# Performance work log

Hardware: AMD Instinct MI355X
Metric: run time of the kernel (lower is better)

## Reference

```python
import jax, jax.numpy as jnp
import numpy as np

NOISE_STD = 0.05
ALPHA = 0.2
B, T, I, H, O = 64, 1000, 16, 512, 8


def setup_inputs() -> dict:
    key = jax.random.key(0)
    ks = jax.random.split(key, 5)
    x = jax.random.normal(ks[0], (B, T, I), dtype=jnp.float32)
    noise = jax.random.normal(ks[1], (B, T, H), dtype=jnp.float32)
    # parameter init mirrors torch: wi ~ N(0,1), wrec ~ N(0, rho/sqrt(H)), wo ~ N(0, 1/H)
    wi = jax.random.normal(ks[2], (I, H), dtype=jnp.float32)
    si = jnp.ones((I,), dtype=jnp.float32)
    wrec = jax.random.normal(ks[3], (H, H), dtype=jnp.float32) * (1.0 / np.sqrt(H))
    wo = jax.random.normal(ks[4], (H, O), dtype=jnp.float32) * (1.0 / H)
    so = jnp.ones((O,), dtype=jnp.float32)
    h0 = jnp.zeros((H,), dtype=jnp.float32)
    return {"x": x, "noise": noise, "wi": wi, "si": si, "wrec": wrec,
            "wo": wo, "so": so, "h0": h0}


def reference(x, noise, wi, si, wrec, wo, so, h0):
    # proxy params: wi_full = (wi.T * si).T ; wo_full = wo * so
    wi_full = si[:, None] * wi            # (I, H)
    wo_full = wo * so                      # (H, O)
    # input projection is time-parallel; hoist out of the scan
    x_proj = jnp.einsum('bti,ih->bth', x, wi_full)  # (B, T, H)

    def step(h, inp):
        xp, nz = inp                       # (B, H) each
        r = jnp.tanh(h)
        h_new = h + NOISE_STD * nz + ALPHA * (-h + r @ wrec.T + xp)
        out_t = jnp.tanh(h_new) @ wo_full  # (B, O)
        return h_new, out_t

    h_init = jnp.broadcast_to(h0, (x.shape[0], h0.shape[0]))
    _, out = jax.lax.scan(step, h_init,
                          (jnp.swapaxes(x_proj, 0, 1), jnp.swapaxes(noise, 0, 1)))
    return jnp.swapaxes(out, 0, 1)         # (B, T, O)
```

## Files before the change

kernel.cpp:

```cpp
#include <hip/hip_runtime.h>

#define BB 64
#define TT 1000
#define II 16
#define HH 512
#define OO 8
#define NOISE_STD 0.05f
#define ALPHA 0.2f

#define NGROUPS 32
#define BPG 2
#define NSLABS 8
#define JS 64
#define NTHREADS 512
#define NBLOCKS (NGROUPS * NSLABS)


__global__ void __launch_bounds__(NTHREADS, 1) rnn_kernel(
    const float* __restrict__ x, const float* __restrict__ noise,
    const float* __restrict__ wi, const float* __restrict__ si,
    const float* __restrict__ wrec, const float* __restrict__ wo,
    const float* __restrict__ so, const float* __restrict__ h0,
    float* __restrict__ out, unsigned long long* rtag)
{
    __shared__ __align__(16) float rlds[2][BPG][HH];
    __shared__ __align__(16) float zpart[2][NSLABS][BPG][JS];
    __shared__ __align__(16) float xpbuf[2][BPG][JS];

    const int tid  = threadIdx.x;
    const int lane = tid & 63;
    const int wid  = tid >> 6;

    const int xcd  = blockIdx.x & 7;
    const int bidx = blockIdx.x >> 3;
    const int grp  = xcd * 4 + (bidx >> 3);
    const int slab = bidx & 7;
    const int gb   = grp * BPG;
    const int j0   = slab * JS;

    float w_reg[64];
    {
        const float4* wrow = (const float4*)(wrec + (size_t)(j0 + lane) * HH + wid * 64);
        #pragma unroll
        for (int c = 0; c < 16; ++c) {
            float4 v = wrow[c];
            w_reg[4*c+0] = v.x; w_reg[4*c+1] = v.y;
            w_reg[4*c+2] = v.z; w_reg[4*c+3] = v.w;
        }
    }

    float hreg = 0.f;
    if (wid < BPG) hreg = h0[j0 + lane];

    float wiF_r[16];
    if (wid >= 6) {
        #pragma unroll
        for (int i = 0; i < 16; ++i) wiF_r[i] = si[i] * wi[i * HH + j0 + lane];
    }
    float wo_r[8][8];
    if (wid == 4 || wid == 5) {
        float so_[8];
        #pragma unroll
        for (int o = 0; o < 8; ++o) so_[o] = so[o];
        #pragma unroll
        for (int m = 0; m < 8; ++m) {
            const float4* wrow = (const float4*)(wo + (size_t)(lane + 64 * m) * OO);
            float4 wa = wrow[0], wb2 = wrow[1];
            wo_r[m][0] = wa.x  * so_[0]; wo_r[m][1] = wa.y  * so_[1];
            wo_r[m][2] = wa.z  * so_[2]; wo_r[m][3] = wa.w  * so_[3];
            wo_r[m][4] = wb2.x * so_[4]; wo_r[m][5] = wb2.y * so_[5];
            wo_r[m][6] = wb2.z * so_[6]; wo_r[m][7] = wb2.w * so_[7];
        }
    }

    unsigned int rb0, rb1;
    {
        float rv = tanhf(h0[wid * 64 + lane]);
        rb0 = __float_as_uint(rv);
        rb1 = rb0;
        rlds[0][0][wid * 64 + lane] = rv;
        rlds[0][1][wid * 64 + lane] = rv;
    }
    if (wid >= 6) {
        const int b = wid - 6;
        const float4* xb = (const float4*)(x + ((size_t)(gb + b) * TT + 0) * II);
        float4 x0 = xb[0], x1 = xb[1], x2 = xb[2], x3 = xb[3];
        xpbuf[0][b][lane] =
              x0.x*wiF_r[0]  + x0.y*wiF_r[1]  + x0.z*wiF_r[2]  + x0.w*wiF_r[3]
            + x1.x*wiF_r[4]  + x1.y*wiF_r[5]  + x1.z*wiF_r[6]  + x1.w*wiF_r[7]
            + x2.x*wiF_r[8]  + x2.y*wiF_r[9]  + x2.z*wiF_r[10] + x2.w*wiF_r[11]
            + x3.x*wiF_r[12] + x3.y*wiF_r[13] + x3.z*wiF_r[14] + x3.w*wiF_r[15];
    }
    __syncthreads();

    for (int t = 0; t < TT; ++t) {
        const int par = t & 1;
        const int nxt = (t + 1) & 1;

        float nz = 0.f;
        if (wid < BPG)
            nz = noise[((size_t)(gb + wid) * TT + t) * HH + j0 + lane];

        if (t > 0) {
            const unsigned long long* s0 =
                rtag + (size_t)par * (BB * HH) + (size_t)gb * HH + wid * 64 + lane;
            unsigned long long v0, v1;
            const unsigned int tg = (unsigned int)t;
            do {
                v0 = __hip_atomic_load(s0,      __ATOMIC_RELAXED, __HIP_MEMORY_SCOPE_AGENT);
                v1 = __hip_atomic_load(s0 + HH, __ATOMIC_RELAXED, __HIP_MEMORY_SCOPE_AGENT);
            } while ((unsigned int)(v0 >> 32) != tg || (unsigned int)(v1 >> 32) != tg);
            rb0 = (unsigned int)v0;
            rb1 = (unsigned int)v1;
            rlds[par][0][wid * 64 + lane] = __uint_as_float(rb0);
            rlds[par][1][wid * 64 + lane] = __uint_as_float(rb1);
        }

        float a0 = 0.f, a1 = 0.f;
        #pragma unroll
        for (int c = 0; c < 64; ++c) {
            float r0 = __uint_as_float(__builtin_amdgcn_readlane(rb0, c));
            float r1 = __uint_as_float(__builtin_amdgcn_readlane(rb1, c));
            a0 += w_reg[c] * r0;
            a1 += w_reg[c] * r1;
        }
        zpart[par][wid][0][lane] = a0;
        zpart[par][wid][1][lane] = a1;
        __syncthreads();

        if (wid < BPG) {
            float z = 0.f;
            #pragma unroll
            for (int k8 = 0; k8 < 8; ++k8) z += zpart[par][k8][wid][lane];
            float xp = xpbuf[par][wid][lane];
            float hn = hreg + NOISE_STD * nz + ALPHA * (z + xp - hreg);
            hreg = hn;
            float rnew = tanhf(hn);
            unsigned long long pv =
                ((unsigned long long)(unsigned int)(t + 1) << 32)
              | (unsigned long long)__float_as_uint(rnew);
            __hip_atomic_store(rtag + (size_t)nxt * (BB * HH)
                                    + (size_t)(gb + wid) * HH + j0 + lane,
                               pv, __ATOMIC_RELAXED, __HIP_MEMORY_SCOPE_AGENT);
        } else if (wid == 4 || wid == 5) {
            const int b = wid - 4;
            if (t > 0) {
                float acc0=0.f,acc1=0.f,acc2=0.f,acc3=0.f,
                      acc4=0.f,acc5=0.f,acc6=0.f,acc7=0.f;
                #pragma unroll
                for (int m = 0; m < 8; ++m) {
                    float rv = rlds[par][b][lane + 64 * m];
                    acc0 += rv * wo_r[m][0]; acc1 += rv * wo_r[m][1];
                    acc2 += rv * wo_r[m][2]; acc3 += rv * wo_r[m][3];
                    acc4 += rv * wo_r[m][4]; acc5 += rv * wo_r[m][5];
                    acc6 += rv * wo_r[m][6]; acc7 += rv * wo_r[m][7];
                }
                float res = 0.f;
                #define RED_(A, O) { float v_ = A; \
                    v_ += __shfl_xor(v_, 1);  v_ += __shfl_xor(v_, 2); \
                    v_ += __shfl_xor(v_, 4);  v_ += __shfl_xor(v_, 8); \
                    v_ += __shfl_xor(v_, 16); v_ += __shfl_xor(v_, 32); \
                    if (lane == O) res = v_; }
                RED_(acc0, 0) RED_(acc1, 1) RED_(acc2, 2) RED_(acc3, 3)
                RED_(acc4, 4) RED_(acc5, 5) RED_(acc6, 6) RED_(acc7, 7)
                #undef RED_
                if (lane < 8)
                    out[((size_t)(gb + b) * TT + (t - 1)) * OO + lane] = res;
            }
        } else if (wid >= 6) {
            const int b = wid - 6;
            if (t + 1 < TT) {
                const float4* xb =
                    (const float4*)(x + ((size_t)(gb + b) * TT + (t + 1)) * II);
                float4 x0 = xb[0], x1 = xb[1], x2 = xb[2], x3 = xb[3];
                xpbuf[nxt][b][lane] =
                      x0.x*wiF_r[0]  + x0.y*wiF_r[1]  + x0.z*wiF_r[2]  + x0.w*wiF_r[3]
                    + x1.x*wiF_r[4]  + x1.y*wiF_r[5]  + x1.z*wiF_r[6]  + x1.w*wiF_r[7]
                    + x2.x*wiF_r[8]  + x2.y*wiF_r[9]  + x2.z*wiF_r[10] + x2.w*wiF_r[11]
                    + x3.x*wiF_r[12] + x3.y*wiF_r[13] + x3.z*wiF_r[14] + x3.w*wiF_r[15];
            }
        }
    }

    {
        const unsigned long long* s0 =
            rtag + (size_t)gb * HH + wid * 64 + lane;
        unsigned long long v0, v1;
        const unsigned int tg = (unsigned int)TT;
        do {
            v0 = __hip_atomic_load(s0,      __ATOMIC_RELAXED, __HIP_MEMORY_SCOPE_AGENT);
            v1 = __hip_atomic_load(s0 + HH, __ATOMIC_RELAXED, __HIP_MEMORY_SCOPE_AGENT);
        } while ((unsigned int)(v0 >> 32) != tg || (unsigned int)(v1 >> 32) != tg);
        rlds[0][0][wid * 64 + lane] = __uint_as_float((unsigned int)v0);
        rlds[0][1][wid * 64 + lane] = __uint_as_float((unsigned int)v1);
    }
    __syncthreads();
    if (wid == 4 || wid == 5) {
        const int b = wid - 4;
        float acc0=0.f,acc1=0.f,acc2=0.f,acc3=0.f,acc4=0.f,acc5=0.f,acc6=0.f,acc7=0.f;
        #pragma unroll
        for (int m = 0; m < 8; ++m) {
            float rv = rlds[0][b][lane + 64 * m];
            acc0 += rv * wo_r[m][0]; acc1 += rv * wo_r[m][1];
            acc2 += rv * wo_r[m][2]; acc3 += rv * wo_r[m][3];
            acc4 += rv * wo_r[m][4]; acc5 += rv * wo_r[m][5];
            acc6 += rv * wo_r[m][6]; acc7 += rv * wo_r[m][7];
        }
        float res = 0.f;
        #define RED_(A, O) { float v_ = A; \
            v_ += __shfl_xor(v_, 1);  v_ += __shfl_xor(v_, 2); \
            v_ += __shfl_xor(v_, 4);  v_ += __shfl_xor(v_, 8); \
            v_ += __shfl_xor(v_, 16); v_ += __shfl_xor(v_, 32); \
            if (lane == O) res = v_; }
        RED_(acc0, 0) RED_(acc1, 1) RED_(acc2, 2) RED_(acc3, 3)
        RED_(acc4, 4) RED_(acc5, 5) RED_(acc6, 6) RED_(acc7, 7)
        #undef RED_
        if (lane < 8)
            out[((size_t)(gb + b) * TT + (TT - 1)) * OO + lane] = res;
    }
}

extern "C" void kernel_launch(void* const* d_in, const int* in_sizes, int n_in,
                              void* d_out, int out_size, void* d_ws, size_t ws_size,
                              hipStream_t stream) {
    const float* x     = (const float*)d_in[0];
    const float* noise = (const float*)d_in[1];
    const float* wi    = (const float*)d_in[2];
    const float* si    = (const float*)d_in[3];
    const float* wrec  = (const float*)d_in[4];
    const float* wo    = (const float*)d_in[5];
    const float* so    = (const float*)d_in[6];
    const float* h0    = (const float*)d_in[7];
    float* out = (float*)d_out;
    unsigned long long* rtag = (unsigned long long*)d_ws;

    (void)in_sizes; (void)n_in; (void)out_size; (void)ws_size;

    void* args[] = {(void*)&x, (void*)&noise, (void*)&wi, (void*)&si,
                    (void*)&wrec, (void*)&wo, (void*)&so, (void*)&h0,
                    (void*)&out, (void*)&rtag};
    hipLaunchCooperativeKernel((void*)rnn_kernel, dim3(NBLOCKS), dim3(NTHREADS),
                               args, 0, stream);
}
```

Measured before the change: 1.992 ms.

## Mirror tagged state into second buffer polled with sc0 cache-bypass loads

Each producer now writes its tagged tanh value twice: to a second workspace copy with a plain global store and to the original copy with an agent-scope atomic store. Consumers poll the second copy using inline-asm loads with the sc0 bit and fall back to the agent-scope atomic copy every fourth iteration. The aim is to lower the latency of the per-step cross-block handoff by using a cheaper load path for most polls. It adds a second store per element and relies on the visibility semantics of the sc0 loads and plain stores, with the atomic copy as a fallback that bounds how long stale data can delay progress.

```diff
diff --git a/kernel.cpp b/kernel.cpp
--- a/kernel.cpp
+++ b/kernel.cpp
@@ -21,7 +21,7 @@
     const float* __restrict__ wi, const float* __restrict__ si,
     const float* __restrict__ wrec, const float* __restrict__ wo,
     const float* __restrict__ so, const float* __restrict__ h0,
-    float* __restrict__ out, unsigned long long* rtag)
+    float* __restrict__ out, unsigned long long* rtagB, unsigned long long* rtagA)
 {
     __shared__ __align__(16) float rlds[2][BPG][HH];
     __shared__ __align__(16) float zpart[2][NSLABS][BPG][JS];
@@ -102,13 +102,26 @@
             nz = noise[((size_t)(gb + wid) * TT + t) * HH + j0 + lane];
 
         if (t > 0) {
-            const unsigned long long* s0 =
-                rtag + (size_t)par * (BB * HH) + (size_t)gb * HH + wid * 64 + lane;
+            const size_t base = (size_t)par * (BB * HH) + (size_t)gb * HH
+                              + wid * 64 + lane;
+            const unsigned long long* sB = rtagB + base;
+            const unsigned long long aA0 = (unsigned long long)(uintptr_t)(rtagA + base);
+            const unsigned long long aA1 = (unsigned long long)(uintptr_t)(rtagA + base + HH);
             unsigned long long v0, v1;
             const unsigned int tg = (unsigned int)t;
+            int it = 0;
             do {
-                v0 = __hip_atomic_load(s0,      __ATOMIC_RELAXED, __HIP_MEMORY_SCOPE_AGENT);
-                v1 = __hip_atomic_load(s0 + HH, __ATOMIC_RELAXED, __HIP_MEMORY_SCOPE_AGENT);
+                if ((it & 3) == 3) {
+                    v0 = __hip_atomic_load(sB,      __ATOMIC_RELAXED, __HIP_MEMORY_SCOPE_AGENT);
+                    v1 = __hip_atomic_load(sB + HH, __ATOMIC_RELAXED, __HIP_MEMORY_SCOPE_AGENT);
+                } else {
+                    asm volatile("global_load_dwordx2 %0, %2, off sc0\n\t"
+                                 "global_load_dwordx2 %1, %3, off sc0\n\t"
+                                 "s_waitcnt vmcnt(0)"
+                                 : "=&v"(v0), "=&v"(v1)
+                                 : "v"(aA0), "v"(aA1) : "memory");
+                }
+                ++it;
             } while ((unsigned int)(v0 >> 32) != tg || (unsigned int)(v1 >> 32) != tg);
             rb0 = (unsigned int)v0;
             rb1 = (unsigned int)v1;
@@ -139,9 +152,13 @@
             unsigned long long pv =
                 ((unsigned long long)(unsigned int)(t + 1) << 32)
               | (unsigned long long)__float_as_uint(rnew);
-            __hip_atomic_store(rtag + (size_t)nxt * (BB * HH)
-                                    + (size_t)(gb + wid) * HH + j0 + lane,
-                               pv, __ATOMIC_RELAXED, __HIP_MEMORY_SCOPE_AGENT);
+            const size_t dbase = (size_t)nxt * (BB * HH)
+                               + (size_t)(gb + wid) * HH + j0 + lane;
+            const unsigned long long adA = (unsigned long long)(uintptr_t)(rtagA + dbase);
+            asm volatile("global_store_dwordx2 %0, %1, off"
+                         :: "v"(adA), "v"(pv) : "memory");
+            __hip_atomic_store(rtagB + dbase, pv, __ATOMIC_RELAXED,
+                               __HIP_MEMORY_SCOPE_AGENT);
         } else if (wid == 4 || wid == 5) {
             const int b = wid - 4;
             if (t > 0) {
@@ -183,13 +200,25 @@
     }
 
     {
-        const unsigned long long* s0 =
-            rtag + (size_t)gb * HH + wid * 64 + lane;
+        const size_t base = (size_t)gb * HH + wid * 64 + lane;
+        const unsigned long long* sB = rtagB + base;
+        const unsigned long long aA0 = (unsigned long long)(uintptr_t)(rtagA + base);
+        const unsigned long long aA1 = (unsigned long long)(uintptr_t)(rtagA + base + HH);
         unsigned long long v0, v1;
         const unsigned int tg = (unsigned int)TT;
+        int it = 0;
         do {
-            v0 = __hip_atomic_load(s0,      __ATOMIC_RELAXED, __HIP_MEMORY_SCOPE_AGENT);
-            v1 = __hip_atomic_load(s0 + HH, __ATOMIC_RELAXED, __HIP_MEMORY_SCOPE_AGENT);
+            if ((it & 3) == 3) {
+                v0 = __hip_atomic_load(sB,      __ATOMIC_RELAXED, __HIP_MEMORY_SCOPE_AGENT);
+                v1 = __hip_atomic_load(sB + HH, __ATOMIC_RELAXED, __HIP_MEMORY_SCOPE_AGENT);
+            } else {
+                asm volatile("global_load_dwordx2 %0, %2, off sc0\n\t"
+                             "global_load_dwordx2 %1, %3, off sc0\n\t"
+                             "s_waitcnt vmcnt(0)"
+                             : "=&v"(v0), "=&v"(v1)
+                             : "v"(aA0), "v"(aA1) : "memory");
+            }
+            ++it;
         } while ((unsigned int)(v0 >> 32) != tg || (unsigned int)(v1 >> 32) != tg);
         rlds[0][0][wid * 64 + lane] = __uint_as_float((unsigned int)v0);
         rlds[0][1][wid * 64 + lane] = __uint_as_float((unsigned int)v1);
@@ -232,13 +261,14 @@
     const float* so    = (const float*)d_in[6];
     const float* h0    = (const float*)d_in[7];
     float* out = (float*)d_out;
-    unsigned long long* rtag = (unsigned long long*)d_ws;
+    unsigned long long* rtagB = (unsigned long long*)d_ws;
+    unsigned long long* rtagA = rtagB + 2 * BB * HH;
 
     (void)in_sizes; (void)n_in; (void)out_size; (void)ws_size;
 
     void* args[] = {(void*)&x, (void*)&noise, (void*)&wi, (void*)&si,
                     (void*)&wrec, (void*)&wo, (void*)&so, (void*)&h0,
-                    (void*)&out, (void*)&rtag};
+                    (void*)&out, (void*)&rtagB, (void*)&rtagA};
     hipLaunchCooperativeKernel((void*)rnn_kernel, dim3(NBLOCKS), dim3(NTHREADS),
                                args, 0, stream);
 }
```

Result: slower. 2.646 ms (+32.8%).

## Pipeline four batch rows per block across staggered sub-steps with warp specialization

Applied to the files above, without the earlier changes.

Each group now handles four batch rows instead of two. Four warps hold 128 wrec columns each and run the matvec for one batch row per sub-step, while four other warps do the state update, input projection and output projection for each row, staggered one sub-step behind. The aim is to overlap the cross-block exchange of the hidden state with useful work on other rows, to prefetch the next row's tagged data, and to replace __syncthreads with a raw s_barrier. This halves the block count and serializes four rows per timestep within a block, so each block runs more barriers per timestep, which could add latency if the overlap does not hide it.

```diff
diff --git a/kernel.cpp b/kernel.cpp
--- a/kernel.cpp
+++ b/kernel.cpp
@@ -8,13 +8,23 @@
 #define NOISE_STD 0.05f
 #define ALPHA 0.2f
 
-#define NGROUPS 32
-#define BPG 2
+#define NGROUPS 16
+#define BPG 4
 #define NSLABS 8
 #define JS 64
 #define NTHREADS 512
 #define NBLOCKS (NGROUPS * NSLABS)
 
+
+#define AGENT_LD(P)   __hip_atomic_load((P), __ATOMIC_RELAXED, __HIP_MEMORY_SCOPE_AGENT)
+#define AGENT_ST(P,V) __hip_atomic_store((P), (V), __ATOMIC_RELAXED, __HIP_MEMORY_SCOPE_AGENT)
+
+#define BAR() do { \
+    asm volatile("s_waitcnt lgkmcnt(0)" ::: "memory"); \
+    __builtin_amdgcn_sched_barrier(0); \
+    __builtin_amdgcn_s_barrier(); \
+    __builtin_amdgcn_sched_barrier(0); \
+} while (0)
 
 __global__ void __launch_bounds__(NTHREADS, 1) rnn_kernel(
     const float* __restrict__ x, const float* __restrict__ noise,
@@ -23,200 +33,199 @@
     const float* __restrict__ so, const float* __restrict__ h0,
     float* __restrict__ out, unsigned long long* rtag)
 {
-    __shared__ __align__(16) float rlds[2][BPG][HH];
-    __shared__ __align__(16) float zpart[2][NSLABS][BPG][JS];
-    __shared__ __align__(16) float xpbuf[2][BPG][JS];
+    __shared__ __align__(16) float zpart[4][4][JS];
+    __shared__ __align__(16) float rlds[4][HH];
 
     const int tid  = threadIdx.x;
     const int lane = tid & 63;
     const int wid  = tid >> 6;
 
     const int xcd  = blockIdx.x & 7;
-    const int bidx = blockIdx.x >> 3;
-    const int grp  = xcd * 4 + (bidx >> 3);
-    const int slab = bidx & 7;
+    const int idx  = blockIdx.x >> 3;
+    const int grp  = xcd * 2 + (idx >> 3);
+    const int slab = idx & 7;
     const int gb   = grp * BPG;
     const int j0   = slab * JS;
 
-    float w_reg[64];
-    {
-        const float4* wrow = (const float4*)(wrec + (size_t)(j0 + lane) * HH + wid * 64);
+    if (wid < 4) {
+        float w_reg[128];
+        {
+            const float4* wrow = (const float4*)(wrec + (size_t)(j0 + lane) * HH + (wid << 7));
+            #pragma unroll
+            for (int c4 = 0; c4 < 32; ++c4) {
+                float4 v = wrow[c4];
+                w_reg[4*c4+0] = v.x; w_reg[4*c4+1] = v.y;
+                w_reg[4*c4+2] = v.z; w_reg[4*c4+3] = v.w;
+            }
+        }
+        const float r0lo = tanhf(h0[(wid << 7) + lane]);
+        const float r0hi = tanhf(h0[(wid << 7) + 64 + lane]);
+        unsigned long long pre0 = 0, pre1 = 0;
+
+        for (int s = 0; s < 4 * TT; ++s) {
+            const int q = s & 3;
+            const int t = s >> 2;
+            float rb0v, rb1v;
+            if (t == 0) { rb0v = r0lo; rb1v = r0hi; }
+            else {
+                const unsigned int tg = (unsigned int)t;
+                unsigned long long v0 = pre0, v1 = pre1;
+                if (((unsigned int)(v0 >> 32) != tg) || ((unsigned int)(v1 >> 32) != tg)) {
+                    const unsigned long long* sp = rtag + (size_t)(t & 1) * (BB * HH)
+                                                  + (size_t)(gb + q) * HH + (wid << 7) + lane;
+                    do { v0 = AGENT_LD(sp); v1 = AGENT_LD(sp + 64); }
+                    while (((unsigned int)(v0 >> 32) != tg) ||
+                           ((unsigned int)(v1 >> 32) != tg));
+                }
+                rb0v = __uint_as_float((unsigned int)v0);
+                rb1v = __uint_as_float((unsigned int)v1);
+            }
+            {
+                const int pn = (q + 1) & 3;
+                const int tn = t + (pn == 0 ? 1 : 0);
+                if (tn >= 1 && tn < TT) {
+                    const unsigned long long* sp = rtag + (size_t)(tn & 1) * (BB * HH)
+                                                  + (size_t)(gb + pn) * HH + (wid << 7) + lane;
+                    pre0 = AGENT_LD(sp);
+                    pre1 = AGENT_LD(sp + 64);
+                }
+            }
+            rlds[q][(wid << 7) + lane]      = rb0v;
+            rlds[q][(wid << 7) + 64 + lane] = rb1v;
+            const unsigned int rbits0 = __float_as_uint(rb0v);
+            const unsigned int rbits1 = __float_as_uint(rb1v);
+            float acc0 = 0.f, acc1 = 0.f;
+            #pragma unroll
+            for (int c = 0; c < 64; ++c) {
+                acc0 += w_reg[c]      * __uint_as_float(__builtin_amdgcn_readlane(rbits0, c));
+                acc1 += w_reg[64 + c] * __uint_as_float(__builtin_amdgcn_readlane(rbits1, c));
+            }
+            zpart[q][wid][lane] = acc0 + acc1;
+            BAR();
+        }
+    } else {
+        const int p = wid - 4;
+        const int b = gb + p;
+        float hreg = h0[j0 + lane];
+        float wiF[16];
         #pragma unroll
-        for (int c = 0; c < 16; ++c) {
-            float4 v = wrow[c];
-            w_reg[4*c+0] = v.x; w_reg[4*c+1] = v.y;
-            w_reg[4*c+2] = v.z; w_reg[4*c+3] = v.w;
-        }
-    }
-
-    float hreg = 0.f;
-    if (wid < BPG) hreg = h0[j0 + lane];
-
-    float wiF_r[16];
-    if (wid >= 6) {
-        #pragma unroll
-        for (int i = 0; i < 16; ++i) wiF_r[i] = si[i] * wi[i * HH + j0 + lane];
-    }
-    float wo_r[8][8];
-    if (wid == 4 || wid == 5) {
-        float so_[8];
-        #pragma unroll
-        for (int o = 0; o < 8; ++o) so_[o] = so[o];
-        #pragma unroll
-        for (int m = 0; m < 8; ++m) {
-            const float4* wrow = (const float4*)(wo + (size_t)(lane + 64 * m) * OO);
-            float4 wa = wrow[0], wb2 = wrow[1];
-            wo_r[m][0] = wa.x  * so_[0]; wo_r[m][1] = wa.y  * so_[1];
-            wo_r[m][2] = wa.z  * so_[2]; wo_r[m][3] = wa.w  * so_[3];
-            wo_r[m][4] = wb2.x * so_[4]; wo_r[m][5] = wb2.y * so_[5];
-            wo_r[m][6] = wb2.z * so_[6]; wo_r[m][7] = wb2.w * so_[7];
-        }
-    }
-
-    unsigned int rb0, rb1;
-    {
-        float rv = tanhf(h0[wid * 64 + lane]);
-        rb0 = __float_as_uint(rv);
-        rb1 = rb0;
-        rlds[0][0][wid * 64 + lane] = rv;
-        rlds[0][1][wid * 64 + lane] = rv;
-    }
-    if (wid >= 6) {
-        const int b = wid - 6;
-        const float4* xb = (const float4*)(x + ((size_t)(gb + b) * TT + 0) * II);
-        float4 x0 = xb[0], x1 = xb[1], x2 = xb[2], x3 = xb[3];
-        xpbuf[0][b][lane] =
-              x0.x*wiF_r[0]  + x0.y*wiF_r[1]  + x0.z*wiF_r[2]  + x0.w*wiF_r[3]
-            + x1.x*wiF_r[4]  + x1.y*wiF_r[5]  + x1.z*wiF_r[6]  + x1.w*wiF_r[7]
-            + x2.x*wiF_r[8]  + x2.y*wiF_r[9]  + x2.z*wiF_r[10] + x2.w*wiF_r[11]
-            + x3.x*wiF_r[12] + x3.y*wiF_r[13] + x3.z*wiF_r[14] + x3.w*wiF_r[15];
-    }
-    __syncthreads();
-
-    for (int t = 0; t < TT; ++t) {
-        const int par = t & 1;
-        const int nxt = (t + 1) & 1;
-
-        float nz = 0.f;
-        if (wid < BPG)
-            nz = noise[((size_t)(gb + wid) * TT + t) * HH + j0 + lane];
-
-        if (t > 0) {
-            const unsigned long long* s0 =
-                rtag + (size_t)par * (BB * HH) + (size_t)gb * HH + wid * 64 + lane;
-            unsigned long long v0, v1;
-            const unsigned int tg = (unsigned int)t;
-            do {
-                v0 = __hip_atomic_load(s0,      __ATOMIC_RELAXED, __HIP_MEMORY_SCOPE_AGENT);
-                v1 = __hip_atomic_load(s0 + HH, __ATOMIC_RELAXED, __HIP_MEMORY_SCOPE_AGENT);
-            } while ((unsigned int)(v0 >> 32) != tg || (unsigned int)(v1 >> 32) != tg);
-            rb0 = (unsigned int)v0;
-            rb1 = (unsigned int)v1;
-            rlds[par][0][wid * 64 + lane] = __uint_as_float(rb0);
-            rlds[par][1][wid * 64 + lane] = __uint_as_float(rb1);
-        }
-
-        float a0 = 0.f, a1 = 0.f;
-        #pragma unroll
-        for (int c = 0; c < 64; ++c) {
-            float r0 = __uint_as_float(__builtin_amdgcn_readlane(rb0, c));
-            float r1 = __uint_as_float(__builtin_amdgcn_readlane(rb1, c));
-            a0 += w_reg[c] * r0;
-            a1 += w_reg[c] * r1;
-        }
-        zpart[par][wid][0][lane] = a0;
-        zpart[par][wid][1][lane] = a1;
-        __syncthreads();
-
-        if (wid < BPG) {
-            float z = 0.f;
-            #pragma unroll
-            for (int k8 = 0; k8 < 8; ++k8) z += zpart[par][k8][wid][lane];
-            float xp = xpbuf[par][wid][lane];
-            float hn = hreg + NOISE_STD * nz + ALPHA * (z + xp - hreg);
-            hreg = hn;
-            float rnew = tanhf(hn);
-            unsigned long long pv =
-                ((unsigned long long)(unsigned int)(t + 1) << 32)
-              | (unsigned long long)__float_as_uint(rnew);
-            __hip_atomic_store(rtag + (size_t)nxt * (BB * HH)
-                                    + (size_t)(gb + wid) * HH + j0 + lane,
-                               pv, __ATOMIC_RELAXED, __HIP_MEMORY_SCOPE_AGENT);
-        } else if (wid == 4 || wid == 5) {
-            const int b = wid - 4;
-            if (t > 0) {
-                float acc0=0.f,acc1=0.f,acc2=0.f,acc3=0.f,
-                      acc4=0.f,acc5=0.f,acc6=0.f,acc7=0.f;
-                #pragma unroll
-                for (int m = 0; m < 8; ++m) {
-                    float rv = rlds[par][b][lane + 64 * m];
-                    acc0 += rv * wo_r[m][0]; acc1 += rv * wo_r[m][1];
-                    acc2 += rv * wo_r[m][2]; acc3 += rv * wo_r[m][3];
-                    acc4 += rv * wo_r[m][4]; acc5 += rv * wo_r[m][5];
-                    acc6 += rv * wo_r[m][6]; acc7 += rv * wo_r[m][7];
-                }
-                float res = 0.f;
-                #define RED_(A, O) { float v_ = A; \
-                    v_ += __shfl_xor(v_, 1);  v_ += __shfl_xor(v_, 2); \
-                    v_ += __shfl_xor(v_, 4);  v_ += __shfl_xor(v_, 8); \
-                    v_ += __shfl_xor(v_, 16); v_ += __shfl_xor(v_, 32); \
-                    if (lane == O) res = v_; }
-                RED_(acc0, 0) RED_(acc1, 1) RED_(acc2, 2) RED_(acc3, 3)
-                RED_(acc4, 4) RED_(acc5, 5) RED_(acc6, 6) RED_(acc7, 7)
-                #undef RED_
-                if (lane < 8)
-                    out[((size_t)(gb + b) * TT + (t - 1)) * OO + lane] = res;
-            }
-        } else if (wid >= 6) {
-            const int b = wid - 6;
-            if (t + 1 < TT) {
-                const float4* xb =
-                    (const float4*)(x + ((size_t)(gb + b) * TT + (t + 1)) * II);
-                float4 x0 = xb[0], x1 = xb[1], x2 = xb[2], x3 = xb[3];
-                xpbuf[nxt][b][lane] =
-                      x0.x*wiF_r[0]  + x0.y*wiF_r[1]  + x0.z*wiF_r[2]  + x0.w*wiF_r[3]
-                    + x1.x*wiF_r[4]  + x1.y*wiF_r[5]  + x1.z*wiF_r[6]  + x1.w*wiF_r[7]
-                    + x2.x*wiF_r[8]  + x2.y*wiF_r[9]  + x2.z*wiF_r[10] + x2.w*wiF_r[11]
-                    + x3.x*wiF_r[12] + x3.y*wiF_r[13] + x3.z*wiF_r[14] + x3.w*wiF_r[15];
-            }
-        }
-    }
-
-    {
-        const unsigned long long* s0 =
-            rtag + (size_t)gb * HH + wid * 64 + lane;
-        unsigned long long v0, v1;
-        const unsigned int tg = (unsigned int)TT;
-        do {
-            v0 = __hip_atomic_load(s0,      __ATOMIC_RELAXED, __HIP_MEMORY_SCOPE_AGENT);
-            v1 = __hip_atomic_load(s0 + HH, __ATOMIC_RELAXED, __HIP_MEMORY_SCOPE_AGENT);
-        } while ((unsigned int)(v0 >> 32) != tg || (unsigned int)(v1 >> 32) != tg);
-        rlds[0][0][wid * 64 + lane] = __uint_as_float((unsigned int)v0);
-        rlds[0][1][wid * 64 + lane] = __uint_as_float((unsigned int)v1);
-    }
-    __syncthreads();
-    if (wid == 4 || wid == 5) {
-        const int b = wid - 4;
-        float acc0=0.f,acc1=0.f,acc2=0.f,acc3=0.f,acc4=0.f,acc5=0.f,acc6=0.f,acc7=0.f;
-        #pragma unroll
-        for (int m = 0; m < 8; ++m) {
-            float rv = rlds[0][b][lane + 64 * m];
-            acc0 += rv * wo_r[m][0]; acc1 += rv * wo_r[m][1];
-            acc2 += rv * wo_r[m][2]; acc3 += rv * wo_r[m][3];
-            acc4 += rv * wo_r[m][4]; acc5 += rv * wo_r[m][5];
-            acc6 += rv * wo_r[m][6]; acc7 += rv * wo_r[m][7];
-        }
-        float res = 0.f;
-        #define RED_(A, O) { float v_ = A; \
+        for (int i = 0; i < II; ++i) wiF[i] = si[i] * wi[i * HH + j0 + lane];
+        float wo_r[8][8];
+        if (slab == p) {
+            float so_[8];
+            #pragma unroll
+            for (int o = 0; o < 8; ++o) so_[o] = so[o];
+            #pragma unroll
+            for (int m = 0; m < 8; ++m) {
+                const float4* wrow = (const float4*)(wo + (size_t)(lane + (m << 6)) * OO);
+                float4 wa = wrow[0], wb2 = wrow[1];
+                wo_r[m][0] = wa.x * so_[0];  wo_r[m][1] = wa.y * so_[1];
+                wo_r[m][2] = wa.z * so_[2];  wo_r[m][3] = wa.w * so_[3];
+                wo_r[m][4] = wb2.x * so_[4]; wo_r[m][5] = wb2.y * so_[5];
+                wo_r[m][6] = wb2.z * so_[6]; wo_r[m][7] = wb2.w * so_[7];
+            }
+        }
+        float nz_cur = noise[((size_t)b * TT + 0) * HH + j0 + lane];
+        float nz_pend = 0.f;
+        float4 xf0, xf1, xf2, xf3;
+        float xp_cur;
+        {
+            const float4* xb = (const float4*)(x + ((size_t)b * TT + 0) * II);
+            float4 a = xb[0], c = xb[1], d = xb[2], e = xb[3];
+            xp_cur = a.x*wiF[0] +a.y*wiF[1] +a.z*wiF[2] +a.w*wiF[3]
+                   + c.x*wiF[4] +c.y*wiF[5] +c.z*wiF[6] +c.w*wiF[7]
+                   + d.x*wiF[8] +d.y*wiF[9] +d.z*wiF[10]+d.w*wiF[11]
+                   + e.x*wiF[12]+e.y*wiF[13]+e.z*wiF[14]+e.w*wiF[15];
+        }
+
+        #define RED_(A, O) { float v_ = (A); \
             v_ += __shfl_xor(v_, 1);  v_ += __shfl_xor(v_, 2); \
             v_ += __shfl_xor(v_, 4);  v_ += __shfl_xor(v_, 8); \
             v_ += __shfl_xor(v_, 16); v_ += __shfl_xor(v_, 32); \
-            if (lane == O) res = v_; }
-        RED_(acc0, 0) RED_(acc1, 1) RED_(acc2, 2) RED_(acc3, 3)
-        RED_(acc4, 4) RED_(acc5, 5) RED_(acc6, 6) RED_(acc7, 7)
+            if (lane == (O)) res = v_; }
+
+        auto do_out = [&](int tau, int slot) {
+            float a0=0,a1=0,a2=0,a3=0,a4=0,a5=0,a6=0,a7=0;
+            #pragma unroll
+            for (int m = 0; m < 8; ++m) {
+                float rv = rlds[slot][lane + (m << 6)];
+                a0 += rv*wo_r[m][0]; a1 += rv*wo_r[m][1]; a2 += rv*wo_r[m][2]; a3 += rv*wo_r[m][3];
+                a4 += rv*wo_r[m][4]; a5 += rv*wo_r[m][5]; a6 += rv*wo_r[m][6]; a7 += rv*wo_r[m][7];
+            }
+            float res = 0.f;
+            RED_(a0,0) RED_(a1,1) RED_(a2,2) RED_(a3,3)
+            RED_(a4,4) RED_(a5,5) RED_(a6,6) RED_(a7,7)
+            if (lane < 8) out[((size_t)b * TT + tau) * OO + lane] = res;
+        };
+
+        for (int s = 0; s < 4 * TT; ++s) {
+            if (s >= 1 && ((s - 1) & 3) == p) {
+                const int td = (s - 1) >> 2;
+                float z = zpart[p][0][lane] + zpart[p][1][lane]
+                        + zpart[p][2][lane] + zpart[p][3][lane];
+                float hn = hreg + NOISE_STD * nz_cur + ALPHA * (z + xp_cur - hreg);
+                hreg = hn;
+                float rnew = tanhf(hn);
+                unsigned long long pv = ((unsigned long long)(unsigned int)(td + 1) << 32)
+                                      | (unsigned long long)__float_as_uint(rnew);
+                AGENT_ST(rtag + (size_t)((td + 1) & 1) * (BB * HH)
+                              + (size_t)b * HH + j0 + lane, pv);
+                if (td + 1 < TT) {
+                    nz_pend = noise[((size_t)b * TT + (td + 1)) * HH + j0 + lane];
+                    const float4* xb = (const float4*)(x + ((size_t)b * TT + (td + 1)) * II);
+                    xf0 = xb[0]; xf1 = xb[1]; xf2 = xb[2]; xf3 = xb[3];
+                }
+            }
+            if (s >= 2 && ((s - 2) & 3) == p) {
+                const int tau = ((s - 2) >> 2) - 1;
+                if (tau >= 0 && slab == p) do_out(tau, p);
+            }
+            if (s >= 3 && ((s - 3) & 3) == p) {
+                const int tnx = ((s - 3) >> 2) + 1;
+                if (tnx < TT) {
+                    xp_cur = xf0.x*wiF[0] +xf0.y*wiF[1] +xf0.z*wiF[2] +xf0.w*wiF[3]
+                           + xf1.x*wiF[4] +xf1.y*wiF[5] +xf1.z*wiF[6] +xf1.w*wiF[7]
+                           + xf2.x*wiF[8] +xf2.y*wiF[9] +xf2.z*wiF[10]+xf2.w*wiF[11]
+                           + xf3.x*wiF[12]+xf3.y*wiF[13]+xf3.z*wiF[14]+xf3.w*wiF[15];
+                    nz_cur = nz_pend;
+                }
+            }
+            BAR();
+        }
+        if (p == 3) {
+            float z = zpart[3][0][lane] + zpart[3][1][lane]
+                    + zpart[3][2][lane] + zpart[3][3][lane];
+            float hn = hreg + NOISE_STD * nz_cur + ALPHA * (z + xp_cur - hreg);
+            float rnew = tanhf(hn);
+            unsigned long long pv = ((unsigned long long)(unsigned int)TT << 32)
+                                  | (unsigned long long)__float_as_uint(rnew);
+            AGENT_ST(rtag + (size_t)(TT & 1) * (BB * HH) + (size_t)b * HH + j0 + lane, pv);
+        }
+        if (slab == p) {
+            if (p >= 2) do_out(TT - 2, p);
+            float rv[8];
+            const unsigned long long* sp =
+                rtag + (size_t)(TT & 1) * (BB * HH) + (size_t)b * HH + lane;
+            #pragma unroll
+            for (int m = 0; m < 8; ++m) {
+                unsigned long long v;
+                do { v = AGENT_LD(sp + (m << 6)); }
+                while ((unsigned int)(v >> 32) != (unsigned int)TT);
+                rv[m] = __uint_as_float((unsigned int)v);
+            }
+            float a0=0,a1=0,a2=0,a3=0,a4=0,a5=0,a6=0,a7=0;
+            #pragma unroll
+            for (int m = 0; m < 8; ++m) {
+                float rvm = rv[m];
+                a0 += rvm*wo_r[m][0]; a1 += rvm*wo_r[m][1]; a2 += rvm*wo_r[m][2]; a3 += rvm*wo_r[m][3];
+                a4 += rvm*wo_r[m][4]; a5 += rvm*wo_r[m][5]; a6 += rvm*wo_r[m][6]; a7 += rvm*wo_r[m][7];
+            }
+            float res = 0.f;
+            RED_(a0,0) RED_(a1,1) RED_(a2,2) RED_(a3,3)
+            RED_(a4,4) RED_(a5,5) RED_(a6,6) RED_(a7,7)
+            if (lane < 8) out[((size_t)b * TT + (TT - 1)) * OO + lane] = res;
+        }
         #undef RED_
-        if (lane < 8)
-            out[((size_t)(gb + b) * TT + (TT - 1)) * OO + lane] = res;
     }
 }
 
```

Measured after the change: 3.056 ms. 1.53x slower.

## Pipeline spin-wait loads and offload noise/x prefetch to helper waves

Applied to the files above, without the earlier changes.

Replaces the serial spin loop on the tagged recurrent-state buffer with three staggered in-flight atomic loads per slot, checked wave-uniformly with __all, to cut the latency of each poll round. The noise and next-step x loads move from the critical update waves to waves 2-3, which are issued before the spin wait and passed through a new LDS buffer. This takes global-load latency off the h-update waves on the per-step critical path, at the cost of extra polling traffic and one more shared buffer.

```diff
diff --git a/kernel.cpp b/kernel.cpp
--- a/kernel.cpp
+++ b/kernel.cpp
@@ -15,6 +15,8 @@
 #define NTHREADS 512
 #define NBLOCKS (NGROUPS * NSLABS)
 
+
+#define AGENT_ST(P,V) __hip_atomic_store((P), (V), __ATOMIC_RELAXED, __HIP_MEMORY_SCOPE_AGENT)
 
 __global__ void __launch_bounds__(NTHREADS, 1) rnn_kernel(
     const float* __restrict__ x, const float* __restrict__ noise,
@@ -26,6 +28,7 @@
     __shared__ __align__(16) float rlds[2][BPG][HH];
     __shared__ __align__(16) float zpart[2][NSLABS][BPG][JS];
     __shared__ __align__(16) float xpbuf[2][BPG][JS];
+    __shared__ __align__(16) float nzbuf[2][BPG][JS];
 
     const int tid  = threadIdx.x;
     const int lane = tid & 63;
@@ -53,7 +56,7 @@
     if (wid < BPG) hreg = h0[j0 + lane];
 
     float wiF_r[16];
-    if (wid >= 6) {
+    if (wid == 2 || wid == 3) {
         #pragma unroll
         for (int i = 0; i < 16; ++i) wiF_r[i] = si[i] * wi[i * HH + j0 + lane];
     }
@@ -81,8 +84,8 @@
         rlds[0][0][wid * 64 + lane] = rv;
         rlds[0][1][wid * 64 + lane] = rv;
     }
-    if (wid >= 6) {
-        const int b = wid - 6;
+    if (wid == 2 || wid == 3) {
+        const int b = wid - 2;
         const float4* xb = (const float4*)(x + ((size_t)(gb + b) * TT + 0) * II);
         float4 x0 = xb[0], x1 = xb[1], x2 = xb[2], x3 = xb[3];
         xpbuf[0][b][lane] =
@@ -97,21 +100,46 @@
         const int par = t & 1;
         const int nxt = (t + 1) & 1;
 
-        float nz = 0.f;
-        if (wid < BPG)
-            nz = noise[((size_t)(gb + wid) * TT + t) * HH + j0 + lane];
+        float nzld = 0.f;
+        float4 xf0, xf1, xf2, xf3;
+        if (wid == 2 || wid == 3) {
+            const int b = wid - 2;
+            nzld = noise[((size_t)(gb + b) * TT + t) * HH + j0 + lane];
+            if (t + 1 < TT) {
+                const float4* xb = (const float4*)(x + ((size_t)(gb + b) * TT + (t + 1)) * II);
+                xf0 = xb[0]; xf1 = xb[1]; xf2 = xb[2]; xf3 = xb[3];
+            }
+        }
 
         if (t > 0) {
             const unsigned long long* s0 =
                 rtag + (size_t)par * (BB * HH) + (size_t)gb * HH + wid * 64 + lane;
-            unsigned long long v0, v1;
+            const unsigned long long* s1 = s0 + HH;
             const unsigned int tg = (unsigned int)t;
-            do {
-                v0 = __hip_atomic_load(s0,      __ATOMIC_RELAXED, __HIP_MEMORY_SCOPE_AGENT);
-                v1 = __hip_atomic_load(s0 + HH, __ATOMIC_RELAXED, __HIP_MEMORY_SCOPE_AGENT);
-            } while ((unsigned int)(v0 >> 32) != tg || (unsigned int)(v1 >> 32) != tg);
-            rb0 = (unsigned int)v0;
-            rb1 = (unsigned int)v1;
+            #define LD0_ __hip_atomic_load(s0, __ATOMIC_RELAXED, __HIP_MEMORY_SCOPE_AGENT)
+            #define LD1_ __hip_atomic_load(s1, __ATOMIC_RELAXED, __HIP_MEMORY_SCOPE_AGENT)
+            unsigned long long pa0 = LD0_, pa1 = LD1_;
+            unsigned long long pb0 = LD0_, pb1 = LD1_;
+            unsigned long long pc0 = LD0_, pc1 = LD1_;
+            unsigned long long r0v, r1v;
+            for (;;) {
+                bool ok = ((unsigned int)(pa0 >> 32) == tg) &
+                          ((unsigned int)(pa1 >> 32) == tg);
+                if (__all(ok)) { r0v = pa0; r1v = pa1; break; }
+                pa0 = LD0_; pa1 = LD1_;
+                ok = ((unsigned int)(pb0 >> 32) == tg) &
+                     ((unsigned int)(pb1 >> 32) == tg);
+                if (__all(ok)) { r0v = pb0; r1v = pb1; break; }
+                pb0 = LD0_; pb1 = LD1_;
+                ok = ((unsigned int)(pc0 >> 32) == tg) &
+                     ((unsigned int)(pc1 >> 32) == tg);
+                if (__all(ok)) { r0v = pc0; r1v = pc1; break; }
+                pc0 = LD0_; pc1 = LD1_;
+            }
+            #undef LD0_
+            #undef LD1_
+            rb0 = (unsigned int)r0v;
+            rb1 = (unsigned int)r1v;
             rlds[par][0][wid * 64 + lane] = __uint_as_float(rb0);
             rlds[par][1][wid * 64 + lane] = __uint_as_float(rb1);
         }
@@ -126,6 +154,8 @@
         }
         zpart[par][wid][0][lane] = a0;
         zpart[par][wid][1][lane] = a1;
+        if (wid == 2 || wid == 3)
+            nzbuf[par][wid - 2][lane] = nzld;
         __syncthreads();
 
         if (wid < BPG) {
@@ -133,15 +163,24 @@
             #pragma unroll
             for (int k8 = 0; k8 < 8; ++k8) z += zpart[par][k8][wid][lane];
             float xp = xpbuf[par][wid][lane];
+            float nz = nzbuf[par][wid][lane];
             float hn = hreg + NOISE_STD * nz + ALPHA * (z + xp - hreg);
             hreg = hn;
             float rnew = tanhf(hn);
             unsigned long long pv =
                 ((unsigned long long)(unsigned int)(t + 1) << 32)
               | (unsigned long long)__float_as_uint(rnew);
-            __hip_atomic_store(rtag + (size_t)nxt * (BB * HH)
-                                    + (size_t)(gb + wid) * HH + j0 + lane,
-                               pv, __ATOMIC_RELAXED, __HIP_MEMORY_SCOPE_AGENT);
+            AGENT_ST(rtag + (size_t)nxt * (BB * HH)
+                          + (size_t)(gb + wid) * HH + j0 + lane, pv);
+        } else if (wid == 2 || wid == 3) {
+            const int b = wid - 2;
+            if (t + 1 < TT) {
+                xpbuf[nxt][b][lane] =
+                      xf0.x*wiF_r[0]  + xf0.y*wiF_r[1]  + xf0.z*wiF_r[2]  + xf0.w*wiF_r[3]
+                    + xf1.x*wiF_r[4]  + xf1.y*wiF_r[5]  + xf1.z*wiF_r[6]  + xf1.w*wiF_r[7]
+                    + xf2.x*wiF_r[8]  + xf2.y*wiF_r[9]  + xf2.z*wiF_r[10] + xf2.w*wiF_r[11]
+                    + xf3.x*wiF_r[12] + xf3.y*wiF_r[13] + xf3.z*wiF_r[14] + xf3.w*wiF_r[15];
+            }
         } else if (wid == 4 || wid == 5) {
             const int b = wid - 4;
             if (t > 0) {
@@ -167,24 +206,11 @@
                 if (lane < 8)
                     out[((size_t)(gb + b) * TT + (t - 1)) * OO + lane] = res;
             }
-        } else if (wid >= 6) {
-            const int b = wid - 6;
-            if (t + 1 < TT) {
-                const float4* xb =
-                    (const float4*)(x + ((size_t)(gb + b) * TT + (t + 1)) * II);
-                float4 x0 = xb[0], x1 = xb[1], x2 = xb[2], x3 = xb[3];
-                xpbuf[nxt][b][lane] =
-                      x0.x*wiF_r[0]  + x0.y*wiF_r[1]  + x0.z*wiF_r[2]  + x0.w*wiF_r[3]
-                    + x1.x*wiF_r[4]  + x1.y*wiF_r[5]  + x1.z*wiF_r[6]  + x1.w*wiF_r[7]
-                    + x2.x*wiF_r[8]  + x2.y*wiF_r[9]  + x2.z*wiF_r[10] + x2.w*wiF_r[11]
-                    + x3.x*wiF_r[12] + x3.y*wiF_r[13] + x3.z*wiF_r[14] + x3.w*wiF_r[15];
-            }
         }
     }
 
     {
-        const unsigned long long* s0 =
-            rtag + (size_t)gb * HH + wid * 64 + lane;
+        const unsigned long long* s0 = rtag + (size_t)gb * HH + wid * 64 + lane;
         unsigned long long v0, v1;
         const unsigned int tg = (unsigned int)TT;
         do {
```

After: 2.355 ms. +18.2%, slower.
